# Kernel tuning notes

Measured on AMD Instinct MI355X. Metric: run time of the kernel, lower is better.

Reference implementation:

```python
import jax, jax.numpy as jnp
import numpy as np

IN_CHANS = 64
OUT_CHANS = 64
IN_SHAPE = (128, 128)
RADIUS_CUTOFF = 0.03
KERNEL_SHAPE = (3, 4)  # (n_rings, n_phi) -> (3-1)*4+1 = 9 basis functions
EPS = 1e-5
NEG_SLOPE = 0.2


def _disco_basis():
    """Dynamically compile the DISCO filter basis on the (2H, 2W) equidistant grid.

    Returns psi of shape [K, kh, kw] (K=9 hat-function basis filters, including
    quadrature weight hx*hy) plus the pixel radii (Ry, Rx) of the support.
    All static -> constant-folded under jit.
    """
    H2, W2 = 2 * IN_SHAPE[0], 2 * IN_SHAPE[1]
    r_cut = RADIUS_CUTOFF / 2.0
    hy, hx = 1.0 / H2, 1.0 / W2            # normalized grid spacing
    Ry = int(np.ceil(r_cut / hy))
    Rx = int(np.ceil(r_cut / hx))
    dy = np.arange(-Ry, Ry + 1)[:, None] * hy
    dx = np.arange(-Rx, Rx + 1)[None, :] * hx
    r = np.sqrt(dy * dy + dx * dx)
    phi = np.arctan2(dy, dx) % (2.0 * np.pi)
    nr, nphi = KERNEL_SHAPE
    K = (nr - 1) * nphi + 1
    dr = r_cut / (nr - 1)
    dphi = 2.0 * np.pi / nphi
    ik = np.arange(K)[:, None, None]
    ir = np.where(ik > 0, (ik - 1) // nphi + 1, 0)   # radial ring index
    iphi = (ik - 1) % nphi                            # angular index
    # radial hat functions centered at ir*dr, clipped at the cutoff radius
    r_val = np.where((np.abs(r - ir * dr) <= dr) & (r <= r_cut),
                     1.0 - np.abs(r - ir * dr) / dr, 0.0)
    # periodic angular hat functions centered at iphi*dphi
    d_ang = np.abs(phi - iphi * dphi)
    d_ang = np.minimum(d_ang, 2.0 * np.pi - d_ang)
    phi_val = np.where(d_ang <= dphi, 1.0 - d_ang / dphi, 0.0)
    psi = np.where(ik == 0, r_val, r_val * phi_val)   # center basis is isotropic
    psi = psi * (hx * hy)                              # quadrature weight
    return jnp.asarray(psi, jnp.float32), Ry, Rx


def _upsample2x_align_corners(x):
    """Bilinear 2x upsample with align_corners=True, x: [N, C, H, W]."""
    N, C, H, W = x.shape

    def axis(n):
        no = 2 * n
        s = jnp.arange(no, dtype=jnp.float32) * (n - 1) / (no - 1)
        i0 = jnp.floor(s).astype(jnp.int32)
        i1 = jnp.minimum(i0 + 1, n - 1)
        w = (s - i0).astype(x.dtype)
        return i0, i1, w

    y0, y1, wy = axis(H)
    x = x[:, :, y0, :] * (1.0 - wy)[None, None, :, None] + x[:, :, y1, :] * wy[None, None, :, None]
    x0, x1, wx = axis(W)
    x = x[:, :, :, x0] * (1.0 - wx) + x[:, :, :, x1] * wx
    return x


def setup_inputs() -> dict:
    key = jax.random.key(0)
    k1, k2 = jax.random.split(key)
    image = jax.random.normal(k1, (4, IN_CHANS, IN_SHAPE[0], IN_SHAPE[1]), dtype=jnp.float32)
    K = (KERNEL_SHAPE[0] - 1) * KERNEL_SHAPE[1] + 1
    scale = 1.0 / np.sqrt(IN_CHANS * K)
    weight = jax.random.normal(k2, (OUT_CHANS, IN_CHANS, K), dtype=jnp.float32) * scale
    return {"image": image, "weight": weight}


def reference(image, weight):
    x = _upsample2x_align_corners(image)  # [N, Cin, 2H, 2W]
    # 2) DISCO conv: contract learned weights with compiled basis -> dense filter
    psi, Ry, Rx = _disco_basis()          # [K, kh, kw]
    kernel = jnp.einsum('oik,khw->oihw', weight, psi)
    y = jax.lax.conv_general_dilated(
        x, kernel, window_strides=(1, 1),
        padding=[(Ry, Ry), (Rx, Rx)],       # 'constant' zero padding, same size
        dimension_numbers=('NCHW', 'OIHW', 'NCHW'))
    # 3) InstanceNorm2d (affine=False, biased variance, eps=1e-5)
    mu = jnp.mean(y, axis=(2, 3), keepdims=True)
    var = jnp.var(y, axis=(2, 3), keepdims=True)
    y = (y - mu) * jax.lax.rsqrt(var + EPS)
    # 4) LeakyReLU(0.2)
    return jnp.where(y >= 0, y, NEG_SLOPE * y)
```

## Files before the change

### kernel.cpp

```cpp
#include <hip/hip_runtime.h>

#define NB 4
#define CIN 64
#define COUT 64
#define H 128
#define W 128
#define H2 256
#define W2 256
#define HSX 23
#define ZS 40

#define WS_W    0
#define WS_P1   32768
#define WS_P2   98304
#define WS_MU   163840
#define WS_RSTD 164096

constexpr double csqrt(double x) {
    double g = x > 1.0 ? x : 1.0;
    for (int i = 0; i < 64; ++i) g = 0.5 * (g + x / g);
    return g;
}
constexpr double catan_pos(double x) {
    double f = 1.0;
    for (int i = 0; i < 6; ++i) { x = x / (1.0 + csqrt(1.0 + x * x)); f *= 2.0; }
    double x2 = x * x, s = 0.0, term = x;
    for (int n = 0; n < 10; ++n) { s += term / (2 * n + 1) * ((n & 1) ? -1.0 : 1.0); term *= x2; }
    return f * s;
}
constexpr double catan2c(double y, double x) {
    const double PI = 3.141592653589793;
    if (x == 0.0 && y == 0.0) return 0.0;
    double ax = x < 0 ? -x : x, ay = y < 0 ? -y : y;
    double a = (ax >= ay) ? catan_pos(ay / ax) : (PI / 2.0 - catan_pos(ax / ay));
    if (x < 0) a = PI - a;
    return (y < 0) ? -a : a;
}

struct PsiTab { double v[81][9]; };
constexpr PsiTab compute_psi() {
    PsiTab P{};
    const double hy = 1.0 / 256.0;
    const double rcut = 0.015;
    const double dr = 0.0075;
    const double PI = 3.141592653589793;
    const double TWO_PI = 6.283185307179586;
    const double dphi = PI / 2.0;
    for (int ky = 0; ky < 9; ++ky)
        for (int kx = 0; kx < 9; ++kx) {
            double dy = (double)(ky - 4) * hy;
            double dx = (double)(kx - 4) * hy;
            double r = csqrt(dy * dy + dx * dx);
            double phi = catan2c(dy, dx);
            if (phi < 0.0) phi += TWO_PI;
            for (int k = 0; k < 9; ++k) {
                int ir = (k == 0) ? 0 : ((k - 1) / 4 + 1);
                double ctr = ir * dr;
                double ad = r > ctr ? r - ctr : ctr - r;
                double rv = (ad <= dr && r <= rcut) ? 1.0 - ad / dr : 0.0;
                double val;
                if (k == 0) val = rv;
                else {
                    int ip = (k - 1) % 4;
                    double da = phi - ip * dphi; if (da < 0) da = -da;
                    double d2 = TWO_PI - da; if (d2 < da) da = d2;
                    double pv = (da <= dphi) ? 1.0 - da / dphi : 0.0;
                    val = rv * pv;
                }
                P.v[ky * 9 + kx][k] = val * (hy * hy);
            }
        }
    return P;
}

struct TapTab {
    int nt;
    int off[48];
    float val[48][9];
    bool nz[48][9];
};
constexpr TapTab make_taps() {
    TapTab T{};
    PsiTab P = compute_psi();
    for (int ky = 0; ky < 9; ++ky)
        for (int kx = 0; kx < 9; ++kx) {
            int t = ky * 9 + kx;
            bool any = false;
            for (int k = 0; k < 9; ++k) if (P.v[t][k] != 0.0) any = true;
            if (!any) continue;
            int dy = ky - 4, dx = kx - 4;
            T.off[T.nt] = dy * HSX + dx;
            for (int k = 0; k < 9; ++k) {
                T.val[T.nt][k] = (float)P.v[t][k];
                T.nz[T.nt][k] = (P.v[t][k] != 0.0);
            }
            T.nt++;
        }
    return T;
}
constexpr TapTab TT = make_taps();
constexpr int NT = TT.nt;
static_assert(NT > 0 && NT <= 48, "tap table overflow");

using f32x2  = __attribute__((ext_vector_type(2))) float;
using f32x4  = __attribute__((ext_vector_type(4))) float;
using bf16x8 = __attribute__((ext_vector_type(8))) short;

__device__ __forceinline__ unsigned short f2bf_rne(float f) {
    unsigned u = __float_as_uint(f);
    unsigned r = (u + 0x7fff + ((u >> 16) & 1)) >> 16;
    return (unsigned short)r;
}
__device__ __forceinline__ unsigned pkrtz(float a, float b) {
    return (__float_as_uint(a) >> 16) | (__float_as_uint(b) & 0xffff0000u);
}

__global__ void setup_w(const float* __restrict__ wgt, float* __restrict__ ws) {
    unsigned short* wsW = (unsigned short*)(ws + WS_W);
    const int g = blockIdx.x;
    const int t = threadIdx.x;
    const int o = t >> 2;
    const int k0 = (t & 3) * 8;
#pragma unroll
    for (int j = 0; j < 8; ++j) {
        int kk = k0 + j;
        int ch = kk >> 4, k = kk & 15;
        float v = (k < 9) ? wgt[((size_t)o * CIN + 2 * g + ch) * 9 + k] : 0.f;
        wsW[g * 2048 + o * 32 + kk] = f2bf_rne(v);
    }
}

__global__ __launch_bounds__(256, 2) void conv_kernel(const float* __restrict__ img,
                                                      float* __restrict__ out,
                                                      float* __restrict__ ws) {
    __shared__ unsigned short zbuf[256][ZS];
    __shared__ f32x2 halo[2][22 * HSX];
    __shared__ f32x2 coarse[2][14 * 15];
    __shared__ float red1[4][64], red2[4][64];

    const int tid  = threadIdx.x;
    const int bid  = blockIdx.x;
    const int n    = bid >> 8;
    const int tile = bid & 255;
    const int ty0  = (tile >> 4) << 4;
    const int tx0  = (tile & 15) << 4;

    const int r = tid >> 4, c = tid & 15;
    const int hbase = (r + 3) * HSX + (c + 3);
    const int wv  = tid >> 6;
    const int l   = tid & 63;
    const int a16 = l & 15;
    const int kseg = (l >> 4) * 8;

    const unsigned short* wsW = (const unsigned short*)(ws + WS_W);

    {
        uint4* zr = (uint4*)&zbuf[0][0];
#pragma unroll
        for (int j = 0; j < 5; ++j) zr[tid + j * 256] = make_uint4(0, 0, 0, 0);
    }

    const float cs = 0.49803922f;

    int cy0 = (int)floorf((float)(ty0 - 3) * cs); cy0 = min(max(cy0, 0), 114);
    int cx0 = (int)floorf((float)(tx0 - 3) * cs); cx0 = min(max(cx0, 0), 114);

    const bool cok = tid < 196;
    const int ci = tid / 14, cj = tid - ci * 14;
    const int cgoff = (cy0 + ci) * W + (cx0 + cj);
    const int cwidx = ci * 15 + cj;
    float cv0 = 0.f, cv1 = 0.f;

    auto cload = [&](int g) {
        if (cok) {
            const float* b = img + ((size_t)n * CIN + 2 * g) * (H * W) + cgoff;
            cv0 = b[0];
            cv1 = b[H * W];
        }
    };
    auto cwrite = [&](int q) {
        if (cok) coarse[q][cwidx] = (f32x2){cv0, cv1};
    };

    int  fA[2], fDY[2], fDX[2], fHW[2];
    float fFY[2], fFX[2];
    bool fOK[2], fZF[2];
#pragma unroll
    for (int j = 0; j < 2; ++j) {
        int e = tid + j * 256;
        fOK[j] = (e < 484);
        int hy = e / 22, hx = e - hy * 22;
        int uy = ty0 - 3 + hy, ux = tx0 - 3 + hx;
        fZF[j] = ((unsigned)uy >= 256u) || ((unsigned)ux >= 256u);
        float syf = (float)uy * cs;
        float sxf = (float)ux * cs;
        int y0 = (int)floorf(syf);
        int x0 = (int)floorf(sxf);
        fFY[j] = syf - (float)y0;
        fFX[j] = sxf - (float)x0;
        int y0c = min(max(y0, 0), 127), x0c = min(max(x0, 0), 127);
        int y1c = min(y0c + 1, 127),    x1c = min(x0c + 1, 127);
        int ly  = min(max(y0c - cy0, 0), 13), lx  = min(max(x0c - cx0, 0), 13);
        int ly1 = min(max(y1c - cy0, 0), 13), lx1 = min(max(x1c - cx0, 0), 13);
        fA[j]  = ly * 15 + lx;
        fDY[j] = (ly1 - ly) * 15;
        fDX[j] = lx1 - lx;
        fHW[j] = hy * HSX + hx;
    }

    auto fine_build = [&](int q) {
#pragma unroll
        for (int j = 0; j < 2; ++j) {
            if (fOK[j]) {
                const f32x2* cb = &coarse[q][0];
                f32x2 c00 = cb[fA[j]];
                f32x2 c01 = cb[fA[j] + fDX[j]];
                f32x2 c10 = cb[fA[j] + fDY[j]];
                f32x2 c11 = cb[fA[j] + fDY[j] + fDX[j]];
                f32x2 fyv = (f32x2){fFY[j], fFY[j]};
                f32x2 fxv = (f32x2){fFX[j], fFX[j]};
                f32x2 t0 = c00 + fyv * (c10 - c00);
                f32x2 t1 = c01 + fyv * (c11 - c01);
                f32x2 v  = t0 + fxv * (t1 - t0);
                if (fZF[j]) v = (f32x2){0.f, 0.f};
                halo[q][fHW[j]] = v;
            }
        }
    };

    auto zphase = [&](int q) {
        const f32x2* hb = &halo[q][hbase - 72];
        f32x2 z[9];
#pragma unroll
        for (int k = 0; k < 9; ++k) z[k] = (f32x2){0.f, 0.f};
#pragma unroll
        for (int t = 0; t < NT; ++t) {
            f32x2 h = hb[72 + TT.off[t]];
#pragma unroll
            for (int k = 0; k < 9; ++k)
                if (TT.nz[t][k]) z[k] += h * TT.val[t][k];
        }
        unsigned short* zr = &zbuf[tid][0];
        *(uint4*)zr = make_uint4(pkrtz(z[0].x, z[1].x), pkrtz(z[2].x, z[3].x),
                                 pkrtz(z[4].x, z[5].x), pkrtz(z[6].x, z[7].x));
        zr[8] = (unsigned short)(__float_as_uint(z[8].x) >> 16);
        *(uint4*)(zr + 16) = make_uint4(pkrtz(z[0].y, z[1].y), pkrtz(z[2].y, z[3].y),
                                        pkrtz(z[4].y, z[5].y), pkrtz(z[6].y, z[7].y));
        zr[24] = (unsigned short)(__float_as_uint(z[8].y) >> 16);
    };

    f32x4 acc[4][4];
#pragma unroll
    for (int m = 0; m < 4; ++m)
#pragma unroll
        for (int t = 0; t < 4; ++t) acc[m][t] = (f32x4){0.f, 0.f, 0.f, 0.f};

    cload(0);
    cwrite(0);
    __syncthreads();
    fine_build(0);
    cload(1);
    __syncthreads();

#pragma unroll 1
    for (int g = 0; g < 32; ++g) {
        const int p = g & 1;
        zphase(p);
        if (g < 31) cwrite(p ^ 1);
        bf16x8 af[4];
        {
            const unsigned short* wp = wsW + g * 2048 + a16 * 32 + kseg;
#pragma unroll
            for (int m = 0; m < 4; ++m)
                af[m] = *(const bf16x8*)(wp + m * 512);
        }
        __syncthreads();

        union { uint2 q2[2]; bf16x8 v; } bfr[4];
#pragma unroll
        for (int t = 0; t < 4; ++t) {
            const unsigned short* zp = &zbuf[wv * 64 + t * 16 + a16][kseg];
            bfr[t].q2[0] = *(const uint2*)zp;
            bfr[t].q2[1] = *(const uint2*)(zp + 4);
        }
#pragma unroll
        for (int m = 0; m < 4; ++m)
#pragma unroll
            for (int t = 0; t < 4; ++t)
                acc[m][t] = __builtin_amdgcn_mfma_f32_16x16x32_bf16(af[m], bfr[t].v, acc[m][t], 0, 0, 0);

        if (g < 31) fine_build(p ^ 1);
        if (g < 30) cload(g + 2);
        __syncthreads();
    }

#pragma unroll
    for (int m = 0; m < 4; ++m) {
#pragma unroll
        for (int r4 = 0; r4 < 4; ++r4) {
            float s = 0.f, q = 0.f;
#pragma unroll
            for (int t = 0; t < 4; ++t) {
                float v = acc[m][t][r4];
                s += v; q = fmaf(v, v, q);
            }
#pragma unroll
            for (int msk = 1; msk < 16; msk <<= 1) {
                s += __shfl_xor(s, msk);
                q += __shfl_xor(q, msk);
            }
            if (a16 == 0) {
                int o = m * 16 + (l >> 4) * 4 + r4;
                red1[wv][o] = s;
                red2[wv][o] = q;
            }
        }
    }

    const size_t nbase = (size_t)n * COUT * (H2 * W2);
#pragma unroll
    for (int m = 0; m < 4; ++m)
#pragma unroll
        for (int t = 0; t < 4; ++t) {
            int Y = ty0 + wv * 4 + t;
            int X = tx0 + a16;
#pragma unroll
            for (int r4 = 0; r4 < 4; ++r4) {
                int o = m * 16 + (l >> 4) * 4 + r4;
                out[nbase + (size_t)o * (H2 * W2) + Y * W2 + X] = acc[m][t][r4];
            }
        }
    __syncthreads();
    if (tid < 64) {
        float S1 = red1[0][tid] + red1[1][tid] + red1[2][tid] + red1[3][tid];
        float S2 = red2[0][tid] + red2[1][tid] + red2[2][tid] + red2[3][tid];
        ws[WS_P1 + (n * COUT + tid) * 256 + tile] = S1;
        ws[WS_P2 + (n * COUT + tid) * 256 + tile] = S2;
    }
}

__global__ void stats_kernel(float* __restrict__ ws) {
    const int co  = blockIdx.x;
    const int tid = threadIdx.x;
    float s1 = ws[WS_P1 + co * 256 + tid];
    float s2 = ws[WS_P2 + co * 256 + tid];
#pragma unroll
    for (int m = 1; m < 64; m <<= 1) { s1 += __shfl_xor(s1, m); s2 += __shfl_xor(s2, m); }
    __shared__ float r1[4], r2[4];
    if ((tid & 63) == 0) { r1[tid >> 6] = s1; r2[tid >> 6] = s2; }
    __syncthreads();
    if (tid == 0) {
        float S1 = r1[0] + r1[1] + r1[2] + r1[3];
        float S2 = r2[0] + r2[1] + r2[2] + r2[3];
        const float inv = 1.f / 65536.f;
        float mu  = S1 * inv;
        float var = S2 * inv - mu * mu;
        ws[WS_MU + co]   = mu;
        ws[WS_RSTD + co] = 1.f / sqrtf(var + 1e-5f);
    }
}

__global__ void norm_kernel(float* __restrict__ out, const float* __restrict__ ws) {
    const int total = NB * COUT * H2 * W2 / 4;
    for (int idx = blockIdx.x * blockDim.x + threadIdx.x; idx < total;
         idx += gridDim.x * blockDim.x) {
        int co = idx >> 14;
        float mu = ws[WS_MU + co];
        float rs = ws[WS_RSTD + co];
        float4 v = ((float4*)out)[idx];
        float* p = (float*)&v;
#pragma unroll
        for (int j = 0; j < 4; ++j) {
            float t = (p[j] - mu) * rs;
            p[j] = (t >= 0.f) ? t : 0.2f * t;
        }
        ((float4*)out)[idx] = v;
    }
}

extern "C" void kernel_launch(void* const* d_in, const int* in_sizes, int n_in,
                              void* d_out, int out_size, void* d_ws, size_t ws_size,
                              hipStream_t stream) {
    const float* img = (const float*)d_in[0];
    const float* wgt = (const float*)d_in[1];
    float* out = (float*)d_out;
    float* ws  = (float*)d_ws;

    setup_w<<<32, 256, 0, stream>>>(wgt, ws);
    conv_kernel<<<NB * 256, 256, 0, stream>>>(img, out, ws);
    stats_kernel<<<256, 256, 0, stream>>>(ws);
    norm_kernel<<<2048, 256, 0, stream>>>(out, ws);
}
```

Baseline: 163.3 us.

## Double conv tile height to 32 rows and compute two output rows per thread

The conv tile grows from 16x16 to 32x16 pixels, so the grid halves and each block stages a 38-row halo and a 21-row coarse patch. Each thread now computes basis responses for two vertically adjacent pixels that share halo loads, and each wave runs 8 MFMA column tiles with 128-bit B-fragment loads. This is meant to cut redundant halo upsampling and loads and to raise MFMA work per weight fragment. In exchange it doubles accumulator registers and the zbuf LDS footprint, which may lower occupancy, and it leaves only 512 blocks on the device.

After: 197.4 us. 1.21x slower.

```diff
diff --git a/kernel.cpp b/kernel.cpp
--- a/kernel.cpp
+++ b/kernel.cpp
@@ -8,13 +8,16 @@
 #define H2 256
 #define W2 256
 #define HSX 23
+#define HROWS 38
+#define CST 14
+#define CROWS 21
 #define ZS 40
 
 #define WS_W    0
 #define WS_P1   32768
-#define WS_P2   98304
-#define WS_MU   163840
-#define WS_RSTD 164096
+#define WS_P2   65536
+#define WS_MU   98304
+#define WS_RSTD 98560
 
 constexpr double csqrt(double x) {
     double g = x > 1.0 ? x : 1.0;
@@ -73,34 +76,30 @@
     return P;
 }
 
-struct TapTab {
-    int nt;
-    int off[48];
-    float val[48][9];
-    bool nz[48][9];
+struct Psi3 {
+    float val[9][9][9];
+    bool  nz[9][9][9];
+    bool  tapany[8][7];
 };
-constexpr TapTab make_taps() {
-    TapTab T{};
+constexpr Psi3 make_psi3() {
+    Psi3 S{};
     PsiTab P = compute_psi();
     for (int ky = 0; ky < 9; ++ky)
-        for (int kx = 0; kx < 9; ++kx) {
-            int t = ky * 9 + kx;
-            bool any = false;
-            for (int k = 0; k < 9; ++k) if (P.v[t][k] != 0.0) any = true;
-            if (!any) continue;
-            int dy = ky - 4, dx = kx - 4;
-            T.off[T.nt] = dy * HSX + dx;
+        for (int kx = 0; kx < 9; ++kx)
             for (int k = 0; k < 9; ++k) {
-                T.val[T.nt][k] = (float)P.v[t][k];
-                T.nz[T.nt][k] = (P.v[t][k] != 0.0);
-            }
-            T.nt++;
-        }
-    return T;
-}
-constexpr TapTab TT = make_taps();
-constexpr int NT = TT.nt;
-static_assert(NT > 0 && NT <= 48, "tap table overflow");
+                S.val[ky][kx][k] = (float)P.v[ky * 9 + kx][k];
+                S.nz[ky][kx][k]  = (P.v[ky * 9 + kx][k] != 0.0);
+            }
+    for (int dm = -3; dm <= 4; ++dm)
+        for (int dx = -3; dx <= 3; ++dx) {
+            bool a = false;
+            if (dm <= 3)  for (int k = 0; k < 9; ++k) a = a || S.nz[dm + 4][dx + 4][k];
+            if (dm >= -2) for (int k = 0; k < 9; ++k) a = a || S.nz[dm + 3][dx + 4][k];
+            S.tapany[dm + 3][dx + 3] = a;
+        }
+    return S;
+}
+constexpr Psi3 PS3 = make_psi3();
 
 using f32x2  = __attribute__((ext_vector_type(2))) float;
 using f32x4  = __attribute__((ext_vector_type(4))) float;
@@ -133,20 +132,21 @@
 __global__ __launch_bounds__(256, 2) void conv_kernel(const float* __restrict__ img,
                                                       float* __restrict__ out,
                                                       float* __restrict__ ws) {
-    __shared__ unsigned short zbuf[256][ZS];
-    __shared__ f32x2 halo[2][22 * HSX];
-    __shared__ f32x2 coarse[2][14 * 15];
+    __shared__ __align__(16) unsigned short zbuf[512][ZS];
+    __shared__ f32x2 halo[2][HROWS * HSX];
+    __shared__ f32x2 coarse[2][CROWS * CST];
     __shared__ float red1[4][64], red2[4][64];
 
     const int tid  = threadIdx.x;
     const int bid  = blockIdx.x;
-    const int n    = bid >> 8;
-    const int tile = bid & 255;
-    const int ty0  = (tile >> 4) << 4;
+    const int n    = bid >> 7;
+    const int tile = bid & 127;
+    const int ty0  = (tile >> 4) << 5;
     const int tx0  = (tile & 15) << 4;
 
-    const int r = tid >> 4, c = tid & 15;
-    const int hbase = (r + 3) * HSX + (c + 3);
+    const int ry = tid >> 4, c = tid & 15;
+    const int hbase = (2 * ry + 3) * HSX + (c + 3);
+    const int px0 = 32 * ry + c;
     const int wv  = tid >> 6;
     const int l   = tid & 63;
     const int a16 = l & 15;
@@ -157,103 +157,130 @@
     {
         uint4* zr = (uint4*)&zbuf[0][0];
 #pragma unroll
-        for (int j = 0; j < 5; ++j) zr[tid + j * 256] = make_uint4(0, 0, 0, 0);
+        for (int j = 0; j < 10; ++j) zr[tid + j * 256] = make_uint4(0, 0, 0, 0);
     }
 
     const float cs = 0.49803922f;
 
-    int cy0 = (int)floorf((float)(ty0 - 3) * cs); cy0 = min(max(cy0, 0), 114);
-    int cx0 = (int)floorf((float)(tx0 - 3) * cs); cx0 = min(max(cx0, 0), 114);
-
-    const bool cok = tid < 196;
-    const int ci = tid / 14, cj = tid - ci * 14;
-    const int cgoff = (cy0 + ci) * W + (cx0 + cj);
-    const int cwidx = ci * 15 + cj;
-    float cv0 = 0.f, cv1 = 0.f;
-
+    int cy0 = (int)floorf((float)(ty0 - 3) * cs); cy0 = min(max(cy0, 0), 128 - CROWS);
+    int cx0 = (int)floorf((float)(tx0 - 3) * cs); cx0 = min(max(cx0, 0), 128 - 13);
+
+    int cgoff[2];
+    float cv0[2], cv1[2];
+#pragma unroll
+    for (int j = 0; j < 2; ++j) {
+        int e = tid + j * 256;
+        if (e < CROWS * 13) {
+            int ci = e / 13, cj = e - ci * 13;
+            cgoff[j] = (cy0 + ci) * W + (cx0 + cj);
+        }
+    }
     auto cload = [&](int g) {
-        if (cok) {
-            const float* b = img + ((size_t)n * CIN + 2 * g) * (H * W) + cgoff;
-            cv0 = b[0];
-            cv1 = b[H * W];
-        }
+        const float* b = img + ((size_t)n * CIN + 2 * g) * (H * W);
+#pragma unroll
+        for (int j = 0; j < 2; ++j)
+            if (tid < CROWS * 13 - j * 256) {
+                cv0[j] = b[cgoff[j]];
+                cv1[j] = b[cgoff[j] + H * W];
+            }
     };
     auto cwrite = [&](int q) {
-        if (cok) coarse[q][cwidx] = (f32x2){cv0, cv1};
+#pragma unroll
+        for (int j = 0; j < 2; ++j)
+            if (tid < CROWS * 13 - j * 256) {
+                int e = tid + j * 256;
+                int ci = e / 13, cj = e - ci * 13;
+                coarse[q][ci * CST + cj] = (f32x2){cv0[j], cv1[j]};
+            }
     };
 
-    int  fA[2], fDY[2], fDX[2], fHW[2];
-    float fFY[2], fFX[2];
-    bool fOK[2], fZF[2];
-#pragma unroll
-    for (int j = 0; j < 2; ++j) {
+    unsigned fM[4];
+    float fFY[4], fFX[4];
+#pragma unroll
+    for (int j = 0; j < 4; ++j) {
         int e = tid + j * 256;
-        fOK[j] = (e < 484);
-        int hy = e / 22, hx = e - hy * 22;
-        int uy = ty0 - 3 + hy, ux = tx0 - 3 + hx;
-        fZF[j] = ((unsigned)uy >= 256u) || ((unsigned)ux >= 256u);
-        float syf = (float)uy * cs;
-        float sxf = (float)ux * cs;
-        int y0 = (int)floorf(syf);
-        int x0 = (int)floorf(sxf);
-        fFY[j] = syf - (float)y0;
-        fFX[j] = sxf - (float)x0;
-        int y0c = min(max(y0, 0), 127), x0c = min(max(x0, 0), 127);
-        int y1c = min(y0c + 1, 127),    x1c = min(x0c + 1, 127);
-        int ly  = min(max(y0c - cy0, 0), 13), lx  = min(max(x0c - cx0, 0), 13);
-        int ly1 = min(max(y1c - cy0, 0), 13), lx1 = min(max(x1c - cx0, 0), 13);
-        fA[j]  = ly * 15 + lx;
-        fDY[j] = (ly1 - ly) * 15;
-        fDX[j] = lx1 - lx;
-        fHW[j] = hy * HSX + hx;
+        if (e < HROWS * 22) {
+            int hy = e / 22, hx = e - hy * 22;
+            int uy = ty0 - 3 + hy, ux = tx0 - 3 + hx;
+            unsigned zf = (((unsigned)uy >= 256u) || ((unsigned)ux >= 256u)) ? 1u : 0u;
+            float syf = (float)uy * cs;
+            float sxf = (float)ux * cs;
+            int y0 = (int)floorf(syf);
+            int x0 = (int)floorf(sxf);
+            fFY[j] = syf - (float)y0;
+            fFX[j] = sxf - (float)x0;
+            int y0c = min(max(y0, 0), 127), x0c = min(max(x0, 0), 127);
+            int dyo = (min(y0c + 1, 127) - y0c);
+            int dxo = (min(x0c + 1, 127) - x0c);
+            unsigned A = (unsigned)((y0c - cy0) * CST + (x0c - cx0));
+            fM[j] = A | ((unsigned)dxo << 9) | ((unsigned)dyo << 10) | (zf << 11)
+                      | ((unsigned)(hy * HSX + hx) << 12);
+        }
     }
 
     auto fine_build = [&](int q) {
 #pragma unroll
-        for (int j = 0; j < 2; ++j) {
-            if (fOK[j]) {
+        for (int j = 0; j < 4; ++j)
+            if (tid < HROWS * 22 - j * 256) {
+                unsigned m = fM[j];
                 const f32x2* cb = &coarse[q][0];
-                f32x2 c00 = cb[fA[j]];
-                f32x2 c01 = cb[fA[j] + fDX[j]];
-                f32x2 c10 = cb[fA[j] + fDY[j]];
-                f32x2 c11 = cb[fA[j] + fDY[j] + fDX[j]];
+                int A = m & 511;
+                int dxo = (m >> 9) & 1;
+                int dyo = ((m >> 10) & 1) * CST;
+                f32x2 c00 = cb[A],       c01 = cb[A + dxo];
+                f32x2 c10 = cb[A + dyo], c11 = cb[A + dyo + dxo];
                 f32x2 fyv = (f32x2){fFY[j], fFY[j]};
                 f32x2 fxv = (f32x2){fFX[j], fFX[j]};
                 f32x2 t0 = c00 + fyv * (c10 - c00);
                 f32x2 t1 = c01 + fyv * (c11 - c01);
                 f32x2 v  = t0 + fxv * (t1 - t0);
-                if (fZF[j]) v = (f32x2){0.f, 0.f};
-                halo[q][fHW[j]] = v;
-            }
-        }
+                if (m & (1u << 11)) v = (f32x2){0.f, 0.f};
+                halo[q][m >> 12] = v;
+            }
     };
 
     auto zphase = [&](int q) {
         const f32x2* hb = &halo[q][hbase - 72];
-        f32x2 z[9];
-#pragma unroll
-        for (int k = 0; k < 9; ++k) z[k] = (f32x2){0.f, 0.f};
-#pragma unroll
-        for (int t = 0; t < NT; ++t) {
-            f32x2 h = hb[72 + TT.off[t]];
-#pragma unroll
-            for (int k = 0; k < 9; ++k)
-                if (TT.nz[t][k]) z[k] += h * TT.val[t][k];
-        }
-        unsigned short* zr = &zbuf[tid][0];
-        *(uint4*)zr = make_uint4(pkrtz(z[0].x, z[1].x), pkrtz(z[2].x, z[3].x),
-                                 pkrtz(z[4].x, z[5].x), pkrtz(z[6].x, z[7].x));
-        zr[8] = (unsigned short)(__float_as_uint(z[8].x) >> 16);
-        *(uint4*)(zr + 16) = make_uint4(pkrtz(z[0].y, z[1].y), pkrtz(z[2].y, z[3].y),
-                                        pkrtz(z[4].y, z[5].y), pkrtz(z[6].y, z[7].y));
-        zr[24] = (unsigned short)(__float_as_uint(z[8].y) >> 16);
+        f32x2 z0[9], z1[9];
+#pragma unroll
+        for (int k = 0; k < 9; ++k) { z0[k] = (f32x2){0.f, 0.f}; z1[k] = (f32x2){0.f, 0.f}; }
+#pragma unroll
+        for (int dm = -3; dm <= 4; ++dm) {
+#pragma unroll
+            for (int dx = -3; dx <= 3; ++dx) {
+                if (PS3.tapany[dm + 3][dx + 3]) {
+                    f32x2 h = hb[72 + dm * HSX + dx];
+#pragma unroll
+                    for (int k = 0; k < 9; ++k) {
+                        if (dm <= 3 && PS3.nz[dm + 4][dx + 4][k])
+                            z0[k] += h * PS3.val[dm + 4][dx + 4][k];
+                        if (dm >= -2 && PS3.nz[dm + 3][dx + 4][k])
+                            z1[k] += h * PS3.val[dm + 3][dx + 4][k];
+                    }
+                }
+            }
+        }
+        unsigned short* zr0 = &zbuf[px0][0];
+        *(uint4*)zr0 = make_uint4(pkrtz(z0[0].x, z0[1].x), pkrtz(z0[2].x, z0[3].x),
+                                  pkrtz(z0[4].x, z0[5].x), pkrtz(z0[6].x, z0[7].x));
+        zr0[8] = (unsigned short)(__float_as_uint(z0[8].x) >> 16);
+        *(uint4*)(zr0 + 16) = make_uint4(pkrtz(z0[0].y, z0[1].y), pkrtz(z0[2].y, z0[3].y),
+                                         pkrtz(z0[4].y, z0[5].y), pkrtz(z0[6].y, z0[7].y));
+        zr0[24] = (unsigned short)(__float_as_uint(z0[8].y) >> 16);
+        unsigned short* zr1 = &zbuf[px0 + 16][0];
+        *(uint4*)zr1 = make_uint4(pkrtz(z1[0].x, z1[1].x), pkrtz(z1[2].x, z1[3].x),
+                                  pkrtz(z1[4].x, z1[5].x), pkrtz(z1[6].x, z1[7].x));
+        zr1[8] = (unsigned short)(__float_as_uint(z1[8].x) >> 16);
+        *(uint4*)(zr1 + 16) = make_uint4(pkrtz(z1[0].y, z1[1].y), pkrtz(z1[2].y, z1[3].y),
+                                         pkrtz(z1[4].y, z1[5].y), pkrtz(z1[6].y, z1[7].y));
+        zr1[24] = (unsigned short)(__float_as_uint(z1[8].y) >> 16);
     };
 
-    f32x4 acc[4][4];
+    f32x4 acc[4][8];
 #pragma unroll
     for (int m = 0; m < 4; ++m)
 #pragma unroll
-        for (int t = 0; t < 4; ++t) acc[m][t] = (f32x4){0.f, 0.f, 0.f, 0.f};
+        for (int t = 0; t < 8; ++t) acc[m][t] = (f32x4){0.f, 0.f, 0.f, 0.f};
 
     cload(0);
     cwrite(0);
@@ -276,18 +303,14 @@
         }
         __syncthreads();
 
-        union { uint2 q2[2]; bf16x8 v; } bfr[4];
-#pragma unroll
-        for (int t = 0; t < 4; ++t) {
-            const unsigned short* zp = &zbuf[wv * 64 + t * 16 + a16][kseg];
-            bfr[t].q2[0] = *(const uint2*)zp;
-            bfr[t].q2[1] = *(const uint2*)(zp + 4);
-        }
-#pragma unroll
-        for (int m = 0; m < 4; ++m)
-#pragma unroll
-            for (int t = 0; t < 4; ++t)
-                acc[m][t] = __builtin_amdgcn_mfma_f32_16x16x32_bf16(af[m], bfr[t].v, acc[m][t], 0, 0, 0);
+        union { uint4 q4; bf16x8 v; } bfr;
+#pragma unroll
+        for (int t = 0; t < 8; ++t) {
+            bfr.q4 = *(const uint4*)&zbuf[wv * 128 + t * 16 + a16][kseg];
+#pragma unroll
+            for (int m = 0; m < 4; ++m)
+                acc[m][t] = __builtin_amdgcn_mfma_f32_16x16x32_bf16(af[m], bfr.v, acc[m][t], 0, 0, 0);
+        }
 
         if (g < 31) fine_build(p ^ 1);
         if (g < 30) cload(g + 2);
@@ -300,7 +323,7 @@
         for (int r4 = 0; r4 < 4; ++r4) {
             float s = 0.f, q = 0.f;
 #pragma unroll
-            for (int t = 0; t < 4; ++t) {
+            for (int t = 0; t < 8; ++t) {
                 float v = acc[m][t][r4];
                 s += v; q = fmaf(v, v, q);
             }
@@ -321,8 +344,8 @@
 #pragma unroll
     for (int m = 0; m < 4; ++m)
 #pragma unroll
-        for (int t = 0; t < 4; ++t) {
-            int Y = ty0 + wv * 4 + t;
+        for (int t = 0; t < 8; ++t) {
+            int Y = ty0 + wv * 8 + t;
             int X = tx0 + a16;
 #pragma unroll
             for (int r4 = 0; r4 < 4; ++r4) {
@@ -334,27 +357,22 @@
     if (tid < 64) {
         float S1 = red1[0][tid] + red1[1][tid] + red1[2][tid] + red1[3][tid];
         float S2 = red2[0][tid] + red2[1][tid] + red2[2][tid] + red2[3][tid];
-        ws[WS_P1 + (n * COUT + tid) * 256 + tile] = S1;
-        ws[WS_P2 + (n * COUT + tid) * 256 + tile] = S2;
+        ws[WS_P1 + (n * COUT + tid) * 128 + tile] = S1;
+        ws[WS_P2 + (n * COUT + tid) * 128 + tile] = S2;
     }
 }
 
 __global__ void stats_kernel(float* __restrict__ ws) {
-    const int co  = blockIdx.x;
-    const int tid = threadIdx.x;
-    float s1 = ws[WS_P1 + co * 256 + tid];
-    float s2 = ws[WS_P2 + co * 256 + tid];
+    const int co = blockIdx.x;
+    const int t  = threadIdx.x;
+    float s1 = ws[WS_P1 + co * 128 + t] + ws[WS_P1 + co * 128 + t + 64];
+    float s2 = ws[WS_P2 + co * 128 + t] + ws[WS_P2 + co * 128 + t + 64];
 #pragma unroll
     for (int m = 1; m < 64; m <<= 1) { s1 += __shfl_xor(s1, m); s2 += __shfl_xor(s2, m); }
-    __shared__ float r1[4], r2[4];
-    if ((tid & 63) == 0) { r1[tid >> 6] = s1; r2[tid >> 6] = s2; }
-    __syncthreads();
-    if (tid == 0) {
-        float S1 = r1[0] + r1[1] + r1[2] + r1[3];
-        float S2 = r2[0] + r2[1] + r2[2] + r2[3];
+    if (t == 0) {
         const float inv = 1.f / 65536.f;
-        float mu  = S1 * inv;
-        float var = S2 * inv - mu * mu;
+        float mu  = s1 * inv;
+        float var = s2 * inv - mu * mu;
         ws[WS_MU + co]   = mu;
         ws[WS_RSTD + co] = 1.f / sqrtf(var + 1e-5f);
     }
@@ -387,7 +405,7 @@
     float* ws  = (float*)d_ws;
 
     setup_w<<<32, 256, 0, stream>>>(wgt, ws);
-    conv_kernel<<<NB * 256, 256, 0, stream>>>(img, out, ws);
-    stats_kernel<<<256, 256, 0, stream>>>(ws);
+    conv_kernel<<<NB * 128, 256, 0, stream>>>(img, out, ws);
+    stats_kernel<<<256, 64, 0, stream>>>(ws);
     norm_kernel<<<2048, 256, 0, stream>>>(out, ws);
 }
```

## Double-buffer zbuf and software-pipeline stages into one barrier per iteration

Applied to the files above, without the earlier changes.

Doubles the bf16 z-buffer in shared memory and reorganizes the channel-group loop into a skewed pipeline. Each iteration runs the MFMAs for the previous group while computing the next z-phase, coarse write, fine halo build and global prefetch, all separated by a single __syncthreads instead of two. It also packs the per-thread fine-build indices and flags into one bitfield register to relieve register pressure, and replaces paired 8-byte LDS reads of B fragments with one 16-byte read. The cost is more LDS per block, which may affect occupancy, and a deeper prefetch distance.

Measured after the change: 155.5 us. -4.8%, faster.

```diff
diff --git a/kernel.cpp b/kernel.cpp
--- a/kernel.cpp
+++ b/kernel.cpp
@@ -133,7 +133,7 @@
 __global__ __launch_bounds__(256, 2) void conv_kernel(const float* __restrict__ img,
                                                       float* __restrict__ out,
                                                       float* __restrict__ ws) {
-    __shared__ unsigned short zbuf[256][ZS];
+    __shared__ __align__(16) unsigned short zbuf[2][256][ZS];
     __shared__ f32x2 halo[2][22 * HSX];
     __shared__ f32x2 coarse[2][14 * 15];
     __shared__ float red1[4][64], red2[4][64];
@@ -155,9 +155,9 @@
     const unsigned short* wsW = (const unsigned short*)(ws + WS_W);
 
     {
-        uint4* zr = (uint4*)&zbuf[0][0];
-#pragma unroll
-        for (int j = 0; j < 5; ++j) zr[tid + j * 256] = make_uint4(0, 0, 0, 0);
+        uint4* zr = (uint4*)&zbuf[0][0][0];
+#pragma unroll
+        for (int j = 0; j < 10; ++j) zr[tid + j * 256] = make_uint4(0, 0, 0, 0);
     }
 
     const float cs = 0.49803922f;
@@ -182,54 +182,53 @@
         if (cok) coarse[q][cwidx] = (f32x2){cv0, cv1};
     };
 
-    int  fA[2], fDY[2], fDX[2], fHW[2];
+    unsigned fM[2];
     float fFY[2], fFX[2];
-    bool fOK[2], fZF[2];
 #pragma unroll
     for (int j = 0; j < 2; ++j) {
         int e = tid + j * 256;
-        fOK[j] = (e < 484);
-        int hy = e / 22, hx = e - hy * 22;
-        int uy = ty0 - 3 + hy, ux = tx0 - 3 + hx;
-        fZF[j] = ((unsigned)uy >= 256u) || ((unsigned)ux >= 256u);
-        float syf = (float)uy * cs;
-        float sxf = (float)ux * cs;
-        int y0 = (int)floorf(syf);
-        int x0 = (int)floorf(sxf);
-        fFY[j] = syf - (float)y0;
-        fFX[j] = sxf - (float)x0;
-        int y0c = min(max(y0, 0), 127), x0c = min(max(x0, 0), 127);
-        int y1c = min(y0c + 1, 127),    x1c = min(x0c + 1, 127);
-        int ly  = min(max(y0c - cy0, 0), 13), lx  = min(max(x0c - cx0, 0), 13);
-        int ly1 = min(max(y1c - cy0, 0), 13), lx1 = min(max(x1c - cx0, 0), 13);
-        fA[j]  = ly * 15 + lx;
-        fDY[j] = (ly1 - ly) * 15;
-        fDX[j] = lx1 - lx;
-        fHW[j] = hy * HSX + hx;
+        if (e < 484) {
+            int hy = e / 22, hx = e - hy * 22;
+            int uy = ty0 - 3 + hy, ux = tx0 - 3 + hx;
+            unsigned zf = (((unsigned)uy >= 256u) || ((unsigned)ux >= 256u)) ? 1u : 0u;
+            float syf = (float)uy * cs;
+            float sxf = (float)ux * cs;
+            int y0 = (int)floorf(syf);
+            int x0 = (int)floorf(sxf);
+            fFY[j] = syf - (float)y0;
+            fFX[j] = sxf - (float)x0;
+            int y0c = min(max(y0, 0), 127), x0c = min(max(x0, 0), 127);
+            int dyo = min(y0c + 1, 127) - y0c;
+            int dxo = min(x0c + 1, 127) - x0c;
+            unsigned A = (unsigned)((y0c - cy0) * 15 + (x0c - cx0));
+            fM[j] = A | ((unsigned)dxo << 9) | ((unsigned)dyo << 10) | (zf << 11)
+                      | ((unsigned)(hy * HSX + hx) << 12);
+        }
     }
 
     auto fine_build = [&](int q) {
 #pragma unroll
-        for (int j = 0; j < 2; ++j) {
-            if (fOK[j]) {
+        for (int j = 0; j < 2; ++j)
+            if (tid < 484 - j * 256) {
+                unsigned m = fM[j];
                 const f32x2* cb = &coarse[q][0];
-                f32x2 c00 = cb[fA[j]];
-                f32x2 c01 = cb[fA[j] + fDX[j]];
-                f32x2 c10 = cb[fA[j] + fDY[j]];
-                f32x2 c11 = cb[fA[j] + fDY[j] + fDX[j]];
+                int A = m & 511;
+                int dxo = (m >> 9) & 1;
+                int dyo = ((m >> 10) & 1) * 15;
+                f32x2 c00 = cb[A],       c01 = cb[A + dxo];
+                f32x2 c10 = cb[A + dyo], c11 = cb[A + dyo + dxo];
                 f32x2 fyv = (f32x2){fFY[j], fFY[j]};
                 f32x2 fxv = (f32x2){fFX[j], fFX[j]};
                 f32x2 t0 = c00 + fyv * (c10 - c00);
                 f32x2 t1 = c01 + fyv * (c11 - c01);
                 f32x2 v  = t0 + fxv * (t1 - t0);
-                if (fZF[j]) v = (f32x2){0.f, 0.f};
-                halo[q][fHW[j]] = v;
-            }
-        }
+                if (m & (1u << 11)) v = (f32x2){0.f, 0.f};
+                halo[q][m >> 12] = v;
+            }
     };
 
-    auto zphase = [&](int q) {
-        const f32x2* hb = &halo[q][hbase - 72];
+    auto zphase = [&](int p) {
+        const f32x2* hb = &halo[p][hbase - 72];
         f32x2 z[9];
 #pragma unroll
         for (int k = 0; k < 9; ++k) z[k] = (f32x2){0.f, 0.f};
@@ -240,7 +239,7 @@
             for (int k = 0; k < 9; ++k)
                 if (TT.nz[t][k]) z[k] += h * TT.val[t][k];
         }
-        unsigned short* zr = &zbuf[tid][0];
+        unsigned short* zr = &zbuf[p][tid][0];
         *(uint4*)zr = make_uint4(pkrtz(z[0].x, z[1].x), pkrtz(z[2].x, z[3].x),
                                  pkrtz(z[4].x, z[5].x), pkrtz(z[6].x, z[7].x));
         zr[8] = (unsigned short)(__float_as_uint(z[8].x) >> 16);
@@ -255,42 +254,37 @@
 #pragma unroll
         for (int t = 0; t < 4; ++t) acc[m][t] = (f32x4){0.f, 0.f, 0.f, 0.f};
 
-    cload(0);
-    cwrite(0);
+    cload(0); cwrite(0);
     __syncthreads();
     fine_build(0);
     cload(1);
     __syncthreads();
+    cwrite(1);
+    cload(2);
+    __syncthreads();
 
 #pragma unroll 1
-    for (int g = 0; g < 32; ++g) {
-        const int p = g & 1;
-        zphase(p);
-        if (g < 31) cwrite(p ^ 1);
-        bf16x8 af[4];
-        {
-            const unsigned short* wp = wsW + g * 2048 + a16 * 32 + kseg;
+    for (int i = 0; i <= 32; ++i) {
+        if (i >= 1) {
+            const int zp = (i - 1) & 1;
+            bf16x8 af[4];
+            const unsigned short* wp = wsW + (i - 1) * 2048 + a16 * 32 + kseg;
 #pragma unroll
             for (int m = 0; m < 4; ++m)
                 af[m] = *(const bf16x8*)(wp + m * 512);
-        }
-        __syncthreads();
-
-        union { uint2 q2[2]; bf16x8 v; } bfr[4];
-#pragma unroll
-        for (int t = 0; t < 4; ++t) {
-            const unsigned short* zp = &zbuf[wv * 64 + t * 16 + a16][kseg];
-            bfr[t].q2[0] = *(const uint2*)zp;
-            bfr[t].q2[1] = *(const uint2*)(zp + 4);
-        }
-#pragma unroll
-        for (int m = 0; m < 4; ++m)
-#pragma unroll
-            for (int t = 0; t < 4; ++t)
-                acc[m][t] = __builtin_amdgcn_mfma_f32_16x16x32_bf16(af[m], bfr[t].v, acc[m][t], 0, 0, 0);
-
-        if (g < 31) fine_build(p ^ 1);
-        if (g < 30) cload(g + 2);
+            union { uint4 q4; bf16x8 v; } bfr;
+#pragma unroll
+            for (int t = 0; t < 4; ++t) {
+                bfr.q4 = *(const uint4*)&zbuf[zp][wv * 64 + t * 16 + a16][kseg];
+#pragma unroll
+                for (int m = 0; m < 4; ++m)
+                    acc[m][t] = __builtin_amdgcn_mfma_f32_16x16x32_bf16(af[m], bfr.v, acc[m][t], 0, 0, 0);
+            }
+        }
+        if (i < 32)  zphase(i & 1);
+        if (i <= 29) cwrite(i & 1);
+        if (i <= 30) fine_build((i + 1) & 1);
+        if (i <= 28) cload(i + 3);
         __syncthreads();
     }
 
```
